# Performance work log

Hardware: AMD Instinct MI355X
Metric: run time of the kernel (lower is better)

## Reference

```python
import jax, jax.numpy as jnp
import numpy as np

B, T, D, H = 32, 512, 256, 256
E = 2 * H          # attention embed dim
NHEADS = 4
LN_EPS = 1e-5


def _lstm_dir(x, dw, W, bW, U, bU, reverse):
    """One-layer improved LSTM over time. W:[5,D,H] bW:[5,H] U:[5,H,H] bU:[5,H].
    Gate order: i, f, o, c_hat, s."""
    # Precompute input projections for all timesteps (batched GEMM).
    xg = jnp.einsum('bti,gih->btgh', x, W) + bW          # [B,T,5,H]
    if reverse:
        xg = xg[:, ::-1]
        dw = dw[:, ::-1]
    xg_t = jnp.swapaxes(xg, 0, 1)                         # [T,B,5,H]
    dw_t = jnp.swapaxes(dw, 0, 1)                         # [T,B,H]

    def step(carry, inp):
        h, c = carry
        xg_s, dw_s = inp
        g = xg_s + jnp.einsum('bh,gho->bgo', h, U) + bU   # [B,5,H]
        i_t = jax.nn.sigmoid(g[:, 0])
        f_t = jax.nn.sigmoid(g[:, 1])
        o_t = jax.nn.sigmoid(g[:, 2])
        c_hat = jnp.tanh(g[:, 3])
        s_t = jax.nn.sigmoid(g[:, 4]) * dw_s
        c_new = f_t * c + i_t * c_hat * s_t
        h_new = o_t * jnp.tanh(c_new)
        return (h_new, c_new), h_new

    h0 = jnp.zeros((x.shape[0], U.shape[-1]), x.dtype)
    (_, _), hs = jax.lax.scan(step, (h0, h0), (xg_t, dw_t))
    hs = jnp.swapaxes(hs, 0, 1)                           # [B,T,H]
    if reverse:
        hs = hs[:, ::-1]
    return hs


def _mha(x, in_w, in_b, out_w, out_b):
    # torch nn.MultiheadAttention with batch_first=True, self-attention
    qkv = x @ in_w.T + in_b                               # [B,T,3E]
    q, k, v = jnp.split(qkv, 3, axis=-1)
    hd = E // NHEADS
    def heads(a):
        return a.reshape(a.shape[0], a.shape[1], NHEADS, hd).transpose(0, 2, 1, 3)
    q, k, v = heads(q), heads(k), heads(v)                # [B,h,T,hd]
    scores = jnp.einsum('bhqd,bhkd->bhqk', q, k) / jnp.sqrt(jnp.asarray(hd, x.dtype))
    attn = jax.nn.softmax(scores, axis=-1)
    o = jnp.einsum('bhqk,bhkd->bhqd', attn, v)            # [B,h,T,hd]
    o = o.transpose(0, 2, 1, 3).reshape(x.shape[0], x.shape[1], E)
    return o @ out_w.T + out_b


def setup_inputs() -> dict:
    key = jax.random.key(0)
    ks = jax.random.split(key, 16)
    s_in = 1.0 / np.sqrt(D)
    s_h = 1.0 / np.sqrt(H)
    s_e = 1.0 / np.sqrt(E)
    return {
        'x': jax.random.normal(ks[0], (B, T, D), jnp.float32),
        'graph_weights': jax.random.uniform(ks[1], (B, T, H), jnp.float32),
        'W_fwd': jax.random.uniform(ks[2], (5, D, H), jnp.float32, -s_in, s_in),
        'bW_fwd': jax.random.uniform(ks[3], (5, H), jnp.float32, -s_in, s_in),
        'U_fwd': jax.random.uniform(ks[4], (5, H, H), jnp.float32, -s_h, s_h),
        'bU_fwd': jax.random.uniform(ks[5], (5, H), jnp.float32, -s_h, s_h),
        'W_bwd': jax.random.uniform(ks[6], (5, D, H), jnp.float32, -s_in, s_in),
        'bW_bwd': jax.random.uniform(ks[7], (5, H), jnp.float32, -s_in, s_in),
        'U_bwd': jax.random.uniform(ks[8], (5, H, H), jnp.float32, -s_h, s_h),
        'bU_bwd': jax.random.uniform(ks[9], (5, H), jnp.float32, -s_h, s_h),
        'in_proj_w': jax.random.uniform(ks[10], (3 * E, E), jnp.float32, -s_e, s_e),
        'in_proj_b': jnp.zeros((3 * E,), jnp.float32),
        'out_proj_w': jax.random.uniform(ks[11], (E, E), jnp.float32, -s_e, s_e),
        'out_proj_b': jnp.zeros((E,), jnp.float32),
        'ln_gamma': jnp.ones((E,), jnp.float32),
        'ln_beta': jnp.zeros((E,), jnp.float32),
    }


def reference(x, graph_weights, W_fwd, bW_fwd, U_fwd, bU_fwd,
              W_bwd, bW_bwd, U_bwd, bU_bwd,
              in_proj_w, in_proj_b, out_proj_w, out_proj_b,
              ln_gamma, ln_beta):
    hf = _lstm_dir(x, graph_weights, W_fwd, bW_fwd, U_fwd, bU_fwd, reverse=False)
    hb = _lstm_dir(x, graph_weights, W_bwd, bW_bwd, U_bwd, bU_bwd, reverse=True)
    out = jnp.concatenate([hf, hb], axis=-1)              # [B,T,2H]
    out = _mha(out, in_proj_w, in_proj_b, out_proj_w, out_proj_b)
    mu = out.mean(-1, keepdims=True)
    var = ((out - mu) ** 2).mean(-1, keepdims=True)
    out = (out - mu) * jax.lax.rsqrt(var + LN_EPS) * ln_gamma + ln_beta
    return out
```

## Files before the change

kernel.cpp:

```cpp
#include <hip/hip_runtime.h>

typedef unsigned int u32;
typedef unsigned short u16;
typedef unsigned long long u64;
typedef float floatx4 __attribute__((ext_vector_type(4)));
typedef int int32x4 __attribute__((ext_vector_type(4)));
typedef __bf16 bf16x8 __attribute__((ext_vector_type(8)));

#define DEV __device__ __forceinline__
#define LOG2E 1.4426950408889634f

DEV u16 f2bf(float f){
  u32 u = __builtin_bit_cast(u32, f);
  u += 0x7FFFu + ((u >> 16) & 1u);
  return (u16)(u >> 16);
}
DEV float bf2f(u16 h){ u32 u = ((u32)h) << 16; return __builtin_bit_cast(float, u); }
DEV u16 f2h_bits(float f){ return __builtin_bit_cast(u16, (_Float16)f); }
DEV float h_bits2f(u16 h){ return (float)__builtin_bit_cast(_Float16, h); }
DEV float exp2n(float x){ float r; asm("v_exp_f32 %0, -%1" : "=v"(r) : "v"(x)); return r; }
DEV float rcp_(float x){ float r; asm("v_rcp_f32 %0, %1" : "=v"(r) : "v"(x)); return r; }
DEV void bar_lds(){
  __builtin_amdgcn_sched_barrier(0);
  asm volatile("s_waitcnt lgkmcnt(0)" ::: "memory");
  __builtin_amdgcn_s_barrier();
  __builtin_amdgcn_sched_barrier(0);
}


__global__ __launch_bounds__(256) void conv_bf16_k(const float* __restrict__ src, u16* __restrict__ dst, int n){
  for (int i = blockIdx.x * 256 + threadIdx.x; i < n; i += gridDim.x * 256)
    dst[i] = f2bf(src[i]);
}

__global__ __launch_bounds__(256) void prep_wt_k(const float* __restrict__ Wf, const float* __restrict__ Wb,
                                                 const float* __restrict__ bWf, const float* __restrict__ bWb,
                                                 const float* __restrict__ bUf, const float* __restrict__ bUb,
                                                 u16* __restrict__ Wt, float* __restrict__ biasWU){
  int idx = blockIdx.x * 256 + threadIdx.x;
  if (idx >= 2560 * 256) return;
  int n = idx >> 8, k = idx & 255;
  int dir = n / 1280, rr = n - dir * 1280, g = rr >> 8, hc = rr & 255;
  const float* W = dir ? Wb : Wf;
  Wt[idx] = f2bf(W[(g * 256 + k) * 256 + hc]);
  if (k == 0)
    biasWU[n] = ((dir ? bWb : bWf)[g * 256 + hc] + (dir ? bUb : bUf)[g * 256 + hc]) * LOG2E;
}

__global__ __launch_bounds__(256) void prep_uq(const float* __restrict__ Uf, const float* __restrict__ Ub,
                                               signed char* __restrict__ ufr, float* __restrict__ cs){
  int colid = blockIdx.x;
  int dir = colid / 1280; int rr = colid - dir * 1280; int g = rr >> 8; int j = rr & 255;
  int k = threadIdx.x;
  const float* U = dir ? Ub : Uf;
  float v = U[((size_t)g * 256 + k) * 256 + j];
  __shared__ float red[256];
  red[k] = fabsf(v); __syncthreads();
  for (int s = 128; s > 0; s >>= 1){ if (k < s) red[k] = fmaxf(red[k], red[k + s]); __syncthreads(); }
  float s = red[0];
  float q = (s > 0.f) ? 127.f / s : 0.f;
  int iq = (int)rintf(v * q);
  int jb = j >> 4, l15 = j & 15;
  int w = jb & 7, jbsel = jb >> 3;
  int c = jbsel * 5 + g;
  int ks = k >> 6, lsub = (k >> 4) & 3, e = k & 15;
  int lane = lsub * 16 + l15;
  ufr[((((size_t)(dir * 8 + w) * 10 + c) * 4 + ks) * 64 + lane) * 16 + e] = (signed char)iq;
  if (k == 0) cs[((size_t)(dir * 8 + w) * 10 + c) * 16 + l15] = (s / 16129.f) * LOG2E;
}

__global__ __launch_bounds__(512) void repack_dw6(const float* __restrict__ dw, floatx4* __restrict__ dwp){
  int blk = blockIdx.x;
  int t_ = blk & 511; int bg = blk >> 9;
  int tid = threadIdx.x;
  int w = tid >> 6, l = tid & 63;
  int l15 = l & 15, l4 = l >> 4;
  int jbL = l4 >> 1, rowH = (l4 & 1) * 4;
  int j = (jbL * 8 + w) * 16 + l15;
  floatx4 o;
  #pragma unroll
  for (int r = 0; r < 4; r++){
    int b = bg * 8 + rowH + r;
    o[r] = dw[((size_t)b * 512 + t_) * 256 + j];
  }
  dwp[(size_t)blk * 512 + tid] = o;
}

__global__ __launch_bounds__(256) void hcat_un6(const u16* __restrict__ hcp, u16* __restrict__ hcat){
  int row = blockIdx.x;
  int b = row >> 9, ts = row & 511;
  int bg = b >> 3, br = b & 7;
  int rv = br & 3;
  int jj = threadIdx.x;
  int jb = jj >> 7, wv = (jj >> 4) & 7, c15 = jj & 15;
  int tidv = wv * 64 + (((jb << 1) | (br >> 2)) * 16) + c15;
  #pragma unroll
  for (int dir = 0; dir < 2; dir++){
    u16 hb = hcp[((((size_t)(dir * 4 + bg) * 512 + ts) * 512 + tidv) << 2) + rv];
    hcat[(size_t)row * 512 + dir * 256 + jj] = f2bf(h_bits2f(hb));
  }
}

__global__ __launch_bounds__(256) void transpose_v_k(const u16* __restrict__ qkv, u16* __restrict__ Vt){
  __shared__ u16 tile[32][33];
  int bh = blockIdx.x, bb = bh >> 2, h = bh & 3;
  int kt0 = blockIdx.y << 5, d0 = blockIdx.z << 5;
  int tx = threadIdx.x, ty = threadIdx.y;
  for (int i = ty; i < 32; i += 8)
    tile[i][tx] = qkv[(size_t)(bb * 512 + kt0 + i) * 1536 + 1024 + h * 128 + d0 + tx];
  __syncthreads();
  for (int i = ty; i < 32; i += 8)
    Vt[((size_t)bh * 128 + d0 + i) * 512 + kt0 + tx] = tile[tx][i];
}


template<int OM>
__global__ __launch_bounds__(256) void gemm_bt(const u16* __restrict__ A, const u16* __restrict__ Bt,
                                               void* __restrict__ C, const float* __restrict__ bias,
                                               int M, int N, int K, int lda, int ldb, int ldc,
                                               long long aB1, long long aB2, long long bB1, long long bB2,
                                               long long cB1, long long cB2, int nb2, float scale){
  int tilesN = N >> 7;
  int bz = blockIdx.y;
  int b1 = bz / nb2, b2 = bz - b1 * nb2;
  const u16* Ab = A + (size_t)(b1 * aB1 + b2 * aB2);
  const u16* Bb = Bt + (size_t)(b1 * bB1 + b2 * bB2);
  size_t cOff = (size_t)(b1 * cB1 + b2 * cB2);
  int tm = blockIdx.x / tilesN, tn = blockIdx.x - tm * tilesN;
  int m0 = tm << 7, n0 = tn << 7;
  __shared__ u16 As[128 * 64];
  __shared__ u16 Bs[128 * 64];
  int t = threadIdx.x;
  int wave = t >> 6, lane = t & 63;
  int wr = wave >> 1, wc = wave & 1;
  int l15 = lane & 15, l4 = lane >> 4;
  floatx4 acc[4][4] = {};
  for (int k0 = 0; k0 < K; k0 += 64){
    #pragma unroll
    for (int i = 0; i < 4; i++){
      int chunk = t + (i << 8);
      int r = chunk >> 3, cx = chunk & 7;
      int sc = ((cx ^ (r & 7)) << 3);
      *(uint4*)(&As[(r << 6) + sc]) = *(const uint4*)(&Ab[(size_t)(m0 + r) * lda + k0 + (cx << 3)]);
      *(uint4*)(&Bs[(r << 6) + sc]) = *(const uint4*)(&Bb[(size_t)(n0 + r) * ldb + k0 + (cx << 3)]);
    }
    __syncthreads();
    #pragma unroll
    for (int kk = 0; kk < 2; kk++){
      bf16x8 af[4], bf[4];
      int co = (kk << 2) + l4;
      #pragma unroll
      for (int mi = 0; mi < 4; mi++){
        int r = (wr << 6) + (mi << 4) + l15;
        af[mi] = __builtin_bit_cast(bf16x8, *(const uint4*)(&As[(r << 6) + ((co ^ (r & 7)) << 3)]));
      }
      #pragma unroll
      for (int ni = 0; ni < 4; ni++){
        int r = (wc << 6) + (ni << 4) + l15;
        bf[ni] = __builtin_bit_cast(bf16x8, *(const uint4*)(&Bs[(r << 6) + ((co ^ (r & 7)) << 3)]));
      }
      #pragma unroll
      for (int mi = 0; mi < 4; mi++)
        #pragma unroll
        for (int ni = 0; ni < 4; ni++)
          acc[mi][ni] = __builtin_amdgcn_mfma_f32_16x16x32_bf16(af[mi], bf[ni], acc[mi][ni], 0, 0, 0);
    }
    __syncthreads();
  }
  #pragma unroll
  for (int mi = 0; mi < 4; mi++){
    int rowb = m0 + (wr << 6) + (mi << 4) + (l4 << 2);
    #pragma unroll
    for (int ni = 0; ni < 4; ni++){
      int col = n0 + (wc << 6) + (ni << 4) + l15;
      float bv = bias ? bias[col] : 0.f;
      #pragma unroll
      for (int r = 0; r < 4; r++){
        float val = acc[mi][ni][r] * scale + bv;
        if (OM == 3){
          int m = rowb + r, n = col;
          int bb2 = m >> 9, tt2 = m & 511;
          int dirX = (n >= 1280) ? 1 : 0;
          int rem = n - dirX * 1280;
          int g2 = rem >> 8, j2 = rem & 255;
          int bg2 = bb2 >> 3, br2 = bb2 & 7;
          int tid2 = ((j2 >> 4) & 7) * 64 + ((((j2 >> 7) << 1) | (br2 >> 2)) << 4) + (j2 & 15);
          size_t idx = ((((size_t)(dirX * 4 + bg2) * 512 + tt2) * 5 + g2) * 512 + tid2) * 4 + (br2 & 3);
          ((u16*)C)[idx] = f2h_bits(val);
        } else {
          size_t off = cOff + (size_t)(rowb + r) * ldc + col;
          if (OM == 0) ((float*)C)[off] = val;
          else if (OM == 1) ((u16*)C)[off] = f2bf(val);
          else ((u16*)C)[off] = f2h_bits(val);
        }
      }
    }
  }
}


#define LSTM_STEP(S, XQC, DVC, XQN, DVN, HRD, HWR)                                         \
{                                                                                          \
  int ts = dir ? (511 - (S)) : (S);                                                        \
  int spc = ((S) + 1) & 511;                                                               \
  int tsn = dir ? (511 - spc) : spc;                                                       \
  _Pragma("unroll")                                                                        \
  for (int g = 0; g < 5; g++)                                                              \
    XQN[g] = xgp[(((size_t)dirbg * 512 + tsn) * 5 + g) * 512 + t];                         \
  DVN = dwp[((size_t)bg * 512 + tsn) * 512 + t];                                           \
  int32x4 a[4];                                                                            \
  _Pragma("unroll")                                                                        \
  for (int ks = 0; ks < 4; ks++){                                                          \
    int kblk = ks * 4 + l4;                                                                \
    a[ks] = *(const int32x4*)&(HRD)[l15 * 256 + ((kblk ^ l15) & 15) * 16];                 \
  }                                                                                        \
  int32x4 accA[5] = {}, accB[5] = {};                                                      \
  _Pragma("unroll")                                                                        \
  for (int g = 0; g < 5; g++)                                                              \
    _Pragma("unroll")                                                                      \
    for (int ks = 0; ks < 4; ks++)                                                         \
      accA[g] = __builtin_amdgcn_mfma_i32_16x16x64_i8(a[ks], uf[g][ks], accA[g], 0, 0, 0); \
  _Pragma("unroll")                                                                        \
  for (int ks = 0; ks < 4; ks++)                                                           \
    accB[0] = __builtin_amdgcn_mfma_i32_16x16x64_i8(a[ks], uf[5][ks], accB[0], 0, 0, 0);   \
  _Pragma("unroll")                                                                        \
  for (int cl = 0; cl < 4; cl++)                                                           \
    _Pragma("unroll")                                                                      \
    for (int ks = 0; ks < 4; ks++){                                                        \
      int32x4 bfr = *(const int32x4*)&uL[(((w * 4 + cl) * 4 + ks) * 64 + l) * 16];         \
      accB[1 + cl] = __builtin_amdgcn_mfma_i32_16x16x64_i8(a[ks], bfr, accB[1 + cl], 0, 0, 0); \
    }                                                                                      \
  _Pragma("unroll")                                                                        \
  for (int g = 0; g < 5; g++)                                                              \
    _Pragma("unroll")                                                                      \
    for (int r = 0; r < 4; r++){                                                           \
      int vbx = __shfl(accB[g][r], l ^ 32, 64);                                            \
      accA[g][r] = hiHalf ? vbx : accA[g][r];                                              \
    }                                                                                      \
  u32 hp0 = 0, hp1 = 0;                                                                    \
  _Pragma("unroll")                                                                        \
  for (int r = 0; r < 4; r++){                                                             \
    float y[5];                                                                            \
    _Pragma("unroll")                                                                      \
    for (int g = 0; g < 5; g++)                                                            \
      y[g] = (float)accA[g][r] * csv5[g] + h_bits2f((u16)(XQC[g] >> (16 * r)));            \
    float ei = exp2n(y[0]), ef = exp2n(y[1]), eo = exp2n(y[2]);                            \
    float ec = exp2n(fmaxf(y[3] + y[3], -100.f));                                          \
    float es = exp2n(y[4]);                                                                \
    float P3 = (1.f + ei) * (1.f + ec) * (1.f + es);                                       \
    float term = (1.f - ec) * DVC[r] * rcp_(P3);                                           \
    cst[r] = cst[r] * rcp_(1.f + ef) + term;                                               \
    float ecc = exp2n(fmaxf(cst[r] * (2.f * LOG2E), -100.f));                              \
    float hv = (1.f - ecc) * rcp_((1.f + eo) * (1.f + ecc));                               \
    u16 h16 = f2h_bits(hv);                                                                \
    if (r < 2){ hp0 |= (u32)h16 << (16 * r); } else { hp1 |= (u32)h16 << (16 * (r - 2)); } \
    int row = rowH + r;                                                                    \
    (HWR)[row * 256 + (((jlane >> 4) ^ row) & 15) * 16 + (jlane & 15)] =                   \
        (signed char)(int)rintf(hv * 127.f);                                               \
  }                                                                                        \
  hcp[((size_t)dirbg * 512 + ts) * 512 + t] = (u64)hp0 | ((u64)hp1 << 32);                 \
  bar_lds();                                                                               \
}

__global__ __launch_bounds__(512, 2) void lstm_rec8(const u64* __restrict__ xgp, const floatx4* __restrict__ dwp,
                                                    const signed char* __restrict__ ufr, const float* __restrict__ cs,
                                                    u64* __restrict__ hcp){
  int dirbg = blockIdx.x;
  int dir = dirbg >> 2, bg = dirbg & 3;
  int t = threadIdx.x;
  int w = t >> 6, l = t & 63;
  int l15 = l & 15, l4 = l >> 4;
  int jbL = l4 >> 1;
  int rowH = (l4 & 1) * 4;
  __shared__ __align__(16) signed char uL[131072];
  __shared__ __align__(16) signed char hB[2][4096];
  ((uint4*)hB)[t] = uint4{0, 0, 0, 0};
  const int32x4* ug = (const int32x4*)ufr;
  size_t ubase = ((size_t)(dir * 8 + w) * 10) * 4 * 64;
  int32x4 uf[6][4];
  #pragma unroll
  for (int c = 0; c < 6; c++)
    #pragma unroll
    for (int ks = 0; ks < 4; ks++)
      uf[c][ks] = ug[ubase + ((size_t)c * 4 + ks) * 64 + l];
  #pragma unroll
  for (int cl = 0; cl < 4; cl++)
    #pragma unroll
    for (int ks = 0; ks < 4; ks++)
      *(int32x4*)&uL[(((w * 4 + cl) * 4 + ks) * 64 + l) * 16] = ug[ubase + ((size_t)(6 + cl) * 4 + ks) * 64 + l];
  float csv5[5];
  #pragma unroll
  for (int g = 0; g < 5; g++)
    csv5[g] = cs[((size_t)(dir * 8 + w) * 10 + jbL * 5 + g) * 16 + l15];
  int jlane = (jbL * 8 + w) * 16 + l15;
  float cst[4] = {0.f, 0.f, 0.f, 0.f};
  int hiHalf = l & 32;
  u64 xqA[5], xqB[5];
  floatx4 dvA, dvB;
  {
    int ts0 = dir ? 511 : 0;
    #pragma unroll
    for (int g = 0; g < 5; g++)
      xqA[g] = xgp[(((size_t)dirbg * 512 + ts0) * 5 + g) * 512 + t];
    dvA = dwp[((size_t)bg * 512 + ts0) * 512 + t];
  }
  __syncthreads();
  for (int s2 = 0; s2 < 512; s2 += 2){
    LSTM_STEP(s2,     xqA, dvA, xqB, dvB, hB[1], hB[0]);
    LSTM_STEP(s2 + 1, xqB, dvB, xqA, dvA, hB[0], hB[1]);
  }
}


__global__ __launch_bounds__(256) void softmax_rows(u16* __restrict__ S){
  int row = blockIdx.x * 4 + (threadIdx.x >> 6);
  int l = threadIdx.x & 63;
  u16* r = S + (size_t)row * 512;
  uint4 v = *(const uint4*)(r + l * 8);
  u32 wsv[4] = {v.x, v.y, v.z, v.w};
  float f[8];
  #pragma unroll
  for (int i = 0; i < 4; i++){
    f[2 * i] = bf2f((u16)(wsv[i] & 0xFFFF));
    f[2 * i + 1] = bf2f((u16)(wsv[i] >> 16));
  }
  float mx = f[0];
  #pragma unroll
  for (int i = 1; i < 8; i++) mx = fmaxf(mx, f[i]);
  for (int m = 1; m < 64; m <<= 1) mx = fmaxf(mx, __shfl_xor(mx, m, 64));
  float e[8], s = 0.f;
  #pragma unroll
  for (int i = 0; i < 8; i++){ e[i] = __expf(f[i] - mx); s += e[i]; }
  for (int m = 1; m < 64; m <<= 1) s += __shfl_xor(s, m, 64);
  float inv = 1.f / s;
  uint4 o;
  u32 ov[4];
  #pragma unroll
  for (int i = 0; i < 4; i++)
    ov[i] = (u32)f2bf(e[2 * i] * inv) | ((u32)f2bf(e[2 * i + 1] * inv) << 16);
  o.x = ov[0]; o.y = ov[1]; o.z = ov[2]; o.w = ov[3];
  *(uint4*)(r + l * 8) = o;
}


__global__ __launch_bounds__(256) void ln_rows(const float* __restrict__ X, const float* __restrict__ g,
                                               const float* __restrict__ be, float* __restrict__ out){
  int row = blockIdx.x * 4 + (threadIdx.x >> 6);
  int l = threadIdx.x & 63;
  const floatx4* p = (const floatx4*)(X + (size_t)row * 512);
  floatx4 aa = p[l * 2], bb = p[l * 2 + 1];
  float v[8];
  #pragma unroll
  for (int i = 0; i < 4; i++){ v[i] = aa[i]; v[4 + i] = bb[i]; }
  float s = 0.f, s2 = 0.f;
  #pragma unroll
  for (int i = 0; i < 8; i++){ s += v[i]; s2 += v[i] * v[i]; }
  for (int m = 1; m < 64; m <<= 1){ s += __shfl_xor(s, m, 64); s2 += __shfl_xor(s2, m, 64); }
  float mu = s * (1.f / 512.f);
  float var = s2 * (1.f / 512.f) - mu * mu;
  float rs = rsqrtf(var + 1e-5f);
  int c0 = l * 8;
  float* orow = out + (size_t)row * 512;
  #pragma unroll
  for (int i = 0; i < 8; i++)
    orow[c0 + i] = (v[i] - mu) * rs * g[c0 + i] + be[c0 + i];
}


extern "C" void kernel_launch(void* const* d_in, const int* in_sizes, int n_in,
                              void* d_out, int out_size, void* d_ws, size_t ws_size,
                              hipStream_t stream){
  (void)in_sizes; (void)n_in; (void)out_size; (void)ws_size;
  const float* x    = (const float*)d_in[0];
  const float* gw   = (const float*)d_in[1];
  const float* Wf   = (const float*)d_in[2];
  const float* bWf  = (const float*)d_in[3];
  const float* Uf   = (const float*)d_in[4];
  const float* bUf  = (const float*)d_in[5];
  const float* Wb   = (const float*)d_in[6];
  const float* bWb  = (const float*)d_in[7];
  const float* Ub   = (const float*)d_in[8];
  const float* bUb  = (const float*)d_in[9];
  const float* inw  = (const float*)d_in[10];
  const float* inb  = (const float*)d_in[11];
  const float* outw = (const float*)d_in[12];
  const float* outb = (const float*)d_in[13];
  const float* gam  = (const float*)d_in[14];
  const float* bet  = (const float*)d_in[15];
  char* ws = (char*)d_ws;

  size_t o = 0;
  auto take = [&](size_t bytes){ size_t r = o; o += (bytes + 255) & ~(size_t)255; return r; };
  size_t o_xb   = take(16384ULL * 256 * 2);
  size_t o_wt   = take(2560ULL * 256 * 2);
  size_t o_bias = take(2560ULL * 4);
  size_t o_inw  = take(1536ULL * 512 * 2);
  size_t o_outw = take(512ULL * 512 * 2);
  size_t o_ufr  = take(655360);
  size_t o_cs   = take(2ULL * 8 * 10 * 16 * 4);
  size_t o_dwp  = take(4ULL * 512 * 512 * 16);
  size_t o_hcp  = take(8ULL * 512 * 512 * 8);
  size_t o_hcat = take(16384ULL * 512 * 2);
  size_t o_xg   = take(16384ULL * 2560 * 2);
  size_t o_vt   = take(128ULL * 128 * 512 * 2);
  size_t o_S    = take(128ULL * 512 * 512 * 2);
  size_t o_qkv  = o_xg;
  size_t o_attn = o_xg + 16384ULL * 1536 * 2;
  size_t o_xgp  = o_xg;
  size_t o_pre  = o_S;

  u16* xb     = (u16*)(ws + o_xb);
  u16* Wt     = (u16*)(ws + o_wt);
  float* bWU  = (float*)(ws + o_bias);
  u16* inwb   = (u16*)(ws + o_inw);
  u16* outwb  = (u16*)(ws + o_outw);
  signed char* ufr = (signed char*)(ws + o_ufr);
  float* cs   = (float*)(ws + o_cs);
  floatx4* dwp = (floatx4*)(ws + o_dwp);
  u64* hcp    = (u64*)(ws + o_hcp);
  u16* hcat   = (u16*)(ws + o_hcat);
  u64* xgp    = (u64*)(ws + o_xgp);
  u16* qkv    = (u16*)(ws + o_qkv);
  u16* attn   = (u16*)(ws + o_attn);
  u16* Vt     = (u16*)(ws + o_vt);
  u16* S      = (u16*)(ws + o_S);
  float* pre  = (float*)(ws + o_pre);

  conv_bf16_k<<<4096, 256, 0, stream>>>(x, xb, 16384 * 256);
  conv_bf16_k<<<1024, 256, 0, stream>>>(inw, inwb, 1536 * 512);
  conv_bf16_k<<<512, 256, 0, stream>>>(outw, outwb, 512 * 512);
  prep_wt_k<<<2560, 256, 0, stream>>>(Wf, Wb, bWf, bWb, bUf, bUb, Wt, bWU);
  prep_uq<<<2560, 256, 0, stream>>>(Uf, Ub, ufr, cs);
  repack_dw6<<<2048, 512, 0, stream>>>(gw, dwp);

  gemm_bt<3><<<dim3(2560, 1), 256, 0, stream>>>(xb, Wt, (void*)xgp, bWU,
      16384, 2560, 256, 256, 256, 2560, 0, 0, 0, 0, 0, 0, 1, LOG2E);

  lstm_rec8<<<8, 512, 0, stream>>>(xgp, dwp, ufr, cs, hcp);

  hcat_un6<<<16384, 256, 0, stream>>>((const u16*)hcp, hcat);

  gemm_bt<1><<<dim3(1536, 1), 256, 0, stream>>>(hcat, inwb, (void*)qkv, inb,
      16384, 1536, 512, 512, 512, 1536, 0, 0, 0, 0, 0, 0, 1, 1.f);

  transpose_v_k<<<dim3(128, 16, 4), dim3(32, 8), 0, stream>>>(qkv, Vt);

  gemm_bt<1><<<dim3(16, 128), 256, 0, stream>>>(qkv, qkv + 512, (void*)S, nullptr,
      512, 512, 128, 1536, 1536, 512,
      786432LL, 128LL, 786432LL, 128LL, 1048576LL, 262144LL, 4, 0.08838834764831845f);

  softmax_rows<<<16384, 256, 0, stream>>>(S);

  gemm_bt<1><<<dim3(4, 128), 256, 0, stream>>>(S, Vt, (void*)attn, nullptr,
      512, 128, 512, 512, 512, 512,
      1048576LL, 262144LL, 262144LL, 65536LL, 262144LL, 128LL, 4, 1.f);

  gemm_bt<0><<<dim3(512, 1), 256, 0, stream>>>(attn, outwb, (void*)pre, outb,
      16384, 512, 512, 512, 512, 512, 0, 0, 0, 0, 0, 0, 1, 1.f);

  ln_rows<<<4096, 256, 0, stream>>>(pre, gam, bet, (float*)d_out);
}
```

Before: 1.051 ms.

## Split LSTM recurrence across 16 blocks with 4 batch rows each

The recurrent LSTM kernel now runs 16 workgroups, each handling 4 batch rows per direction, instead of 8 workgroups with 8 rows. Each lane now owns 2 rows rather than 4. The xg, dw and h buffers and the GEMM epilogue layout are repacked to match, and the old half-swap shuffle is replaced by lane-broadcast shuffles and selects. This spreads the latency-bound sequential recurrence over more compute units so each step does less elementwise work. The cost is that every block still issues the full set of MFMA tiles on mostly padded rows and needs more shuffles.

```diff
diff --git a/kernel.cpp b/kernel.cpp
--- a/kernel.cpp
+++ b/kernel.cpp
@@ -4,6 +4,7 @@
 typedef unsigned short u16;
 typedef unsigned long long u64;
 typedef float floatx4 __attribute__((ext_vector_type(4)));
+typedef float floatx2 __attribute__((ext_vector_type(2)));
 typedef int int32x4 __attribute__((ext_vector_type(4)));
 typedef __bf16 bf16x8 __attribute__((ext_vector_type(8)));
 
@@ -69,34 +70,32 @@
   if (k == 0) cs[((size_t)(dir * 8 + w) * 10 + c) * 16 + l15] = (s / 16129.f) * LOG2E;
 }
 
-__global__ __launch_bounds__(512) void repack_dw6(const float* __restrict__ dw, floatx4* __restrict__ dwp){
+__global__ __launch_bounds__(512) void repack_dw9(const float* __restrict__ dw, floatx2* __restrict__ dwp){
   int blk = blockIdx.x;
   int t_ = blk & 511; int bg = blk >> 9;
   int tid = threadIdx.x;
   int w = tid >> 6, l = tid & 63;
-  int l15 = l & 15, l4 = l >> 4;
-  int jbL = l4 >> 1, rowH = (l4 & 1) * 4;
+  int l15 = l & 15, l4q = l >> 4;
+  int jbL = l4q >> 1, rBase = (l4q & 1) * 2;
   int j = (jbL * 8 + w) * 16 + l15;
-  floatx4 o;
-  #pragma unroll
-  for (int r = 0; r < 4; r++){
-    int b = bg * 8 + rowH + r;
-    o[r] = dw[((size_t)b * 512 + t_) * 256 + j];
-  }
+  floatx2 o;
+  o[0] = dw[((size_t)(bg * 4 + rBase) * 512 + t_) * 256 + j];
+  o[1] = dw[((size_t)(bg * 4 + rBase + 1) * 512 + t_) * 256 + j];
   dwp[(size_t)blk * 512 + tid] = o;
 }
 
-__global__ __launch_bounds__(256) void hcat_un6(const u16* __restrict__ hcp, u16* __restrict__ hcat){
+__global__ __launch_bounds__(256) void hcat_un9(const u16* __restrict__ hcp, u16* __restrict__ hcat){
   int row = blockIdx.x;
   int b = row >> 9, ts = row & 511;
-  int bg = b >> 3, br = b & 7;
-  int rv = br & 3;
+  int bg = b >> 2, br = b & 3;
   int jj = threadIdx.x;
-  int jb = jj >> 7, wv = (jj >> 4) & 7, c15 = jj & 15;
-  int tidv = wv * 64 + (((jb << 1) | (br >> 2)) * 16) + c15;
+  int jbsel = jj >> 7, wv = (jj >> 4) & 7, c15 = jj & 15;
+  int l4q = jbsel * 2 + (br >> 1);
+  int slot = br & 1;
+  int tidv = wv * 64 + l4q * 16 + c15;
   #pragma unroll
   for (int dir = 0; dir < 2; dir++){
-    u16 hb = hcp[((((size_t)(dir * 4 + bg) * 512 + ts) * 512 + tidv) << 2) + rv];
+    u16 hb = hcp[((((size_t)(dir * 8 + bg) * 512 + ts) * 512 + tidv) << 1) + slot];
     hcat[(size_t)row * 512 + dir * 256 + jj] = f2bf(h_bits2f(hb));
   }
 }
@@ -183,9 +182,11 @@
           int dirX = (n >= 1280) ? 1 : 0;
           int rem = n - dirX * 1280;
           int g2 = rem >> 8, j2 = rem & 255;
-          int bg2 = bb2 >> 3, br2 = bb2 & 7;
-          int tid2 = ((j2 >> 4) & 7) * 64 + ((((j2 >> 7) << 1) | (br2 >> 2)) << 4) + (j2 & 15);
-          size_t idx = ((((size_t)(dirX * 4 + bg2) * 512 + tt2) * 5 + g2) * 512 + tid2) * 4 + (br2 & 3);
+          int bg2 = bb2 >> 2, row2 = bb2 & 3;
+          int l4q2 = (j2 >> 7) * 2 + (row2 >> 1);
+          int slot2 = row2 & 1;
+          int tid2 = ((j2 >> 4) & 7) * 64 + l4q2 * 16 + (j2 & 15);
+          size_t idx = (((((size_t)(dirX * 8 + bg2) * 512 + tt2) * 5 + g2) * 512 + tid2) << 1) + slot2;
           ((u16*)C)[idx] = f2h_bits(val);
         } else {
           size_t off = cOff + (size_t)(rowb + r) * ldc + col;
@@ -211,7 +212,7 @@
   int32x4 a[4];                                                                            \
   _Pragma("unroll")                                                                        \
   for (int ks = 0; ks < 4; ks++){                                                          \
-    int kblk = ks * 4 + l4;                                                                \
+    int kblk = ks * 4 + l4q;                                                               \
     a[ks] = *(const int32x4*)&(HRD)[l15 * 256 + ((kblk ^ l15) & 15) * 16];                 \
   }                                                                                        \
   int32x4 accA[5] = {}, accB[5] = {};                                                      \
@@ -230,48 +231,54 @@
       int32x4 bfr = *(const int32x4*)&uL[(((w * 4 + cl) * 4 + ks) * 64 + l) * 16];         \
       accB[1 + cl] = __builtin_amdgcn_mfma_i32_16x16x64_i8(a[ks], bfr, accB[1 + cl], 0, 0, 0); \
     }                                                                                      \
-  _Pragma("unroll")                                                                        \
-  for (int g = 0; g < 5; g++)                                                              \
-    _Pragma("unroll")                                                                      \
-    for (int r = 0; r < 4; r++){                                                           \
-      int vbx = __shfl(accB[g][r], l ^ 32, 64);                                            \
-      accA[g][r] = hiHalf ? vbx : accA[g][r];                                              \
-    }                                                                                      \
-  u32 hp0 = 0, hp1 = 0;                                                                    \
-  _Pragma("unroll")                                                                        \
-  for (int r = 0; r < 4; r++){                                                             \
+  int ys0[5], ys1[5];                                                                      \
+  _Pragma("unroll")                                                                        \
+  for (int g = 0; g < 5; g++){                                                             \
+    int t0 = __shfl(accA[g][0], l15, 64), t1 = __shfl(accA[g][1], l15, 64);                \
+    int t2 = __shfl(accA[g][2], l15, 64), t3 = __shfl(accA[g][3], l15, 64);                \
+    int u0 = __shfl(accB[g][0], l15, 64), u1 = __shfl(accB[g][1], l15, 64);                \
+    int u2 = __shfl(accB[g][2], l15, 64), u3 = __shfl(accB[g][3], l15, 64);                \
+    int p0 = sel1 ? t2 : t0, p1 = sel1 ? t3 : t1;                                          \
+    int q0 = sel1 ? u2 : u0, q1 = sel1 ? u3 : u1;                                          \
+    ys0[g] = jbH ? q0 : p0;                                                                \
+    ys1[g] = jbH ? q1 : p1;                                                                \
+  }                                                                                        \
+  u32 hpck = 0;                                                                            \
+  _Pragma("unroll")                                                                        \
+  for (int s = 0; s < 2; s++){                                                             \
     float y[5];                                                                            \
     _Pragma("unroll")                                                                      \
     for (int g = 0; g < 5; g++)                                                            \
-      y[g] = (float)accA[g][r] * csv5[g] + h_bits2f((u16)(XQC[g] >> (16 * r)));            \
+      y[g] = (float)(s ? ys1[g] : ys0[g]) * csv5[g] + h_bits2f((u16)(XQC[g] >> (16 * s))); \
     float ei = exp2n(y[0]), ef = exp2n(y[1]), eo = exp2n(y[2]);                            \
     float ec = exp2n(fmaxf(y[3] + y[3], -100.f));                                          \
     float es = exp2n(y[4]);                                                                \
     float P3 = (1.f + ei) * (1.f + ec) * (1.f + es);                                       \
-    float term = (1.f - ec) * DVC[r] * rcp_(P3);                                           \
-    cst[r] = cst[r] * rcp_(1.f + ef) + term;                                               \
-    float ecc = exp2n(fmaxf(cst[r] * (2.f * LOG2E), -100.f));                              \
+    float term = (1.f - ec) * DVC[s] * rcp_(P3);                                           \
+    cst[s] = cst[s] * rcp_(1.f + ef) + term;                                               \
+    float ecc = exp2n(fmaxf(cst[s] * (2.f * LOG2E), -100.f));                              \
     float hv = (1.f - ecc) * rcp_((1.f + eo) * (1.f + ecc));                               \
     u16 h16 = f2h_bits(hv);                                                                \
-    if (r < 2){ hp0 |= (u32)h16 << (16 * r); } else { hp1 |= (u32)h16 << (16 * (r - 2)); } \
-    int row = rowH + r;                                                                    \
+    hpck |= (u32)h16 << (16 * s);                                                          \
+    int row = rBase + s;                                                                   \
     (HWR)[row * 256 + (((jlane >> 4) ^ row) & 15) * 16 + (jlane & 15)] =                   \
         (signed char)(int)rintf(hv * 127.f);                                               \
   }                                                                                        \
-  hcp[((size_t)dirbg * 512 + ts) * 512 + t] = (u64)hp0 | ((u64)hp1 << 32);                 \
+  hcp[((size_t)dirbg * 512 + ts) * 512 + t] = hpck;                                        \
   bar_lds();                                                                               \
 }
 
-__global__ __launch_bounds__(512, 2) void lstm_rec8(const u64* __restrict__ xgp, const floatx4* __restrict__ dwp,
+__global__ __launch_bounds__(512, 2) void lstm_rec9(const u32* __restrict__ xgp, const floatx2* __restrict__ dwp,
                                                     const signed char* __restrict__ ufr, const float* __restrict__ cs,
-                                                    u64* __restrict__ hcp){
+                                                    u32* __restrict__ hcp){
   int dirbg = blockIdx.x;
-  int dir = dirbg >> 2, bg = dirbg & 3;
+  int dir = dirbg >> 3, bg = dirbg & 7;
   int t = threadIdx.x;
   int w = t >> 6, l = t & 63;
-  int l15 = l & 15, l4 = l >> 4;
-  int jbL = l4 >> 1;
-  int rowH = (l4 & 1) * 4;
+  int l15 = l & 15, l4q = l >> 4;
+  int jbH = l4q >> 1;
+  int sel1 = l4q & 1;
+  int rBase = sel1 * 2;
   __shared__ __align__(16) signed char uL[131072];
   __shared__ __align__(16) signed char hB[2][4096];
   ((uint4*)hB)[t] = uint4{0, 0, 0, 0};
@@ -291,12 +298,11 @@
   float csv5[5];
   #pragma unroll
   for (int g = 0; g < 5; g++)
-    csv5[g] = cs[((size_t)(dir * 8 + w) * 10 + jbL * 5 + g) * 16 + l15];
-  int jlane = (jbL * 8 + w) * 16 + l15;
-  float cst[4] = {0.f, 0.f, 0.f, 0.f};
-  int hiHalf = l & 32;
-  u64 xqA[5], xqB[5];
-  floatx4 dvA, dvB;
+    csv5[g] = cs[((size_t)(dir * 8 + w) * 10 + jbH * 5 + g) * 16 + l15];
+  int jlane = (jbH * 8 + w) * 16 + l15;
+  float cst[2] = {0.f, 0.f};
+  u32 xqA[5], xqB[5];
+  floatx2 dvA, dvB;
   {
     int ts0 = dir ? 511 : 0;
     #pragma unroll
@@ -398,8 +404,8 @@
   size_t o_outw = take(512ULL * 512 * 2);
   size_t o_ufr  = take(655360);
   size_t o_cs   = take(2ULL * 8 * 10 * 16 * 4);
-  size_t o_dwp  = take(4ULL * 512 * 512 * 16);
-  size_t o_hcp  = take(8ULL * 512 * 512 * 8);
+  size_t o_dwp  = take(8ULL * 512 * 512 * 8);
+  size_t o_hcp  = take(16ULL * 512 * 512 * 4);
   size_t o_hcat = take(16384ULL * 512 * 2);
   size_t o_xg   = take(16384ULL * 2560 * 2);
   size_t o_vt   = take(128ULL * 128 * 512 * 2);
@@ -416,10 +422,10 @@
   u16* outwb  = (u16*)(ws + o_outw);
   signed char* ufr = (signed char*)(ws + o_ufr);
   float* cs   = (float*)(ws + o_cs);
-  floatx4* dwp = (floatx4*)(ws + o_dwp);
-  u64* hcp    = (u64*)(ws + o_hcp);
+  floatx2* dwp = (floatx2*)(ws + o_dwp);
+  u32* hcp    = (u32*)(ws + o_hcp);
   u16* hcat   = (u16*)(ws + o_hcat);
-  u64* xgp    = (u64*)(ws + o_xgp);
+  u32* xgp    = (u32*)(ws + o_xgp);
   u16* qkv    = (u16*)(ws + o_qkv);
   u16* attn   = (u16*)(ws + o_attn);
   u16* Vt     = (u16*)(ws + o_vt);
@@ -431,14 +437,14 @@
   conv_bf16_k<<<512, 256, 0, stream>>>(outw, outwb, 512 * 512);
   prep_wt_k<<<2560, 256, 0, stream>>>(Wf, Wb, bWf, bWb, bUf, bUb, Wt, bWU);
   prep_uq<<<2560, 256, 0, stream>>>(Uf, Ub, ufr, cs);
-  repack_dw6<<<2048, 512, 0, stream>>>(gw, dwp);
+  repack_dw9<<<4096, 512, 0, stream>>>(gw, dwp);
 
   gemm_bt<3><<<dim3(2560, 1), 256, 0, stream>>>(xb, Wt, (void*)xgp, bWU,
       16384, 2560, 256, 256, 256, 2560, 0, 0, 0, 0, 0, 0, 1, LOG2E);
 
-  lstm_rec8<<<8, 512, 0, stream>>>(xgp, dwp, ufr, cs, hcp);
-
-  hcat_un6<<<16384, 256, 0, stream>>>((const u16*)hcp, hcat);
+  lstm_rec9<<<16, 512, 0, stream>>>(xgp, dwp, ufr, cs, hcp);
+
+  hcat_un9<<<16384, 256, 0, stream>>>((const u16*)hcp, hcat);
 
   gemm_bt<1><<<dim3(1536, 1), 256, 0, stream>>>(hcat, inwb, (void*)qkv, inb,
       16384, 1536, 512, 512, 512, 1536, 0, 0, 0, 0, 0, 0, 1, 1.f);
```

Result: slower. 1.105 ms (+5.1%).
